# Kernel tuning notes

Hardware: AMD Instinct MI355X
Metric: run time of the kernel (lower is better)

Reference implementation:

```python
import jax, jax.numpy as jnp
import numpy as np

N_ATOMS = 300000
N_COLS = 8
VOCAB = 4096      # nn.Embedding(4096, per_col_dim)
D_COL = 32        # per_col_dim
HID = 256         # hidden_size
N_BONDS = 320000
B_GRAPHS = 6000
ATOMS_PER_GRAPH = 50
STEPS = 3
SENTINEL = 999999999


def _linear_params(key, fan_in, fan_out):
    lim = 1.0 / np.sqrt(fan_in)
    kw, kb = jax.random.split(key)
    W = jax.random.uniform(kw, (fan_out, fan_in), minval=-lim, maxval=lim, dtype=jnp.float32)
    b = jax.random.uniform(kb, (fan_out,), minval=-lim, maxval=lim, dtype=jnp.float32)
    return W, b


def setup_inputs() -> dict:
    key = jax.random.key(0)
    ks = jax.random.split(key, 8)
    a_features = jax.random.randint(ks[0], (N_ATOMS, N_COLS), 0, VOCAB, dtype=jnp.int32)
    uv = jax.random.randint(ks[1], (N_BONDS, 2), 0, N_ATOMS, dtype=jnp.int32)
    bextra = jax.random.randint(ks[2], (N_BONDS, 1), 0, 16, dtype=jnp.int32)
    b_features = jnp.concatenate([uv, bextra], axis=1)
    # contiguous equal-length scopes: graph i owns atoms [i*50, i*50+50)
    starts = np.arange(B_GRAPHS, dtype=np.int32) * ATOMS_PER_GRAPH
    lengths = np.full(B_GRAPHS, ATOMS_PER_GRAPH, dtype=np.int32)
    a_scopes = jnp.asarray(np.stack([starts, lengths], axis=1))
    emb_weights = jax.random.normal(ks[3], (N_COLS, VOCAB, D_COL), dtype=jnp.float32) * 0.02
    W_in, b_in = _linear_params(ks[4], D_COL, HID)
    W_self, b_self = _linear_params(ks[5], HID, HID)
    W_neigh, b_neigh = _linear_params(ks[6], HID, HID)
    W_out, b_out = _linear_params(ks[7], HID, HID)
    return {
        'a_features': a_features, 'b_features': b_features, 'a_scopes': a_scopes,
        'emb_weights': emb_weights,
        'W_in': W_in, 'b_in': b_in,
        'W_self': W_self, 'b_self': b_self,
        'W_neigh': W_neigh, 'b_neigh': b_neigh,
        'W_out': W_out, 'b_out': b_out,
    }


def reference(a_features, b_features, a_scopes, emb_weights,
              W_in, b_in, W_self, b_self, W_neigh, b_neigh, W_out, b_out):
    # --- per-column embedding lookup, summed over columns ---
    idx = jnp.remainder(a_features, VOCAB)
    idx = jnp.where(a_features >= SENTINEL, 0, idx)          # sentinel -> index 0
    x = jnp.zeros((a_features.shape[0], D_COL), dtype=emb_weights.dtype)
    for c in range(N_COLS):                                   # fixed small loop over columns
        x = x + emb_weights[c][idx[:, c]]
    h = x @ W_in.T + b_in                                     # [N, HID]
    # --- undirected edges -> two directed edge lists ---
    u = b_features[:, 0]
    v = b_features[:, 1]
    src = jnp.concatenate([u, v], axis=0)
    dst = jnp.concatenate([v, u], axis=0)
    # --- message passing steps ---
    for _ in range(STEPS):
        agg = jnp.zeros_like(h).at[dst].add(h[src])           # scatter-add neighbor sum
        h = jax.nn.relu(h @ W_self.T + b_self + agg @ W_neigh.T + b_neigh)
    h = h @ W_out.T + b_out
    # --- per-graph mean pooling over contiguous scopes ---
    lengths = a_scopes[:, 1]
    seg_ids = jnp.repeat(jnp.arange(a_scopes.shape[0]), lengths,
                         total_repeat_length=h.shape[0])
    sums = jax.ops.segment_sum(h, seg_ids, num_segments=a_scopes.shape[0])
    denom = jnp.maximum(lengths, 1).astype(h.dtype)[:, None]
    return sums / denom
```

## Files before the change

### kernel.cpp

```cpp
#include <hip/hip_runtime.h>

#define NATOMS 300000
#define NCOLS 8
#define VOCABSZ 4096
#define DCOL 32
#define HIDDIM 256
#define NBONDS 320000
#define NGRAPHS 6000
#define NSTEPS 3

constexpr int MP = 300032;
constexpr int MTILES64 = MP / 64;

typedef _Float16 f16;
typedef _Float16 f16x4 __attribute__((ext_vector_type(4)));
typedef _Float16 f16x8 __attribute__((ext_vector_type(8)));
typedef float f32x4 __attribute__((ext_vector_type(4)));

constexpr float LO_SCALE = 2048.0f;
constexpr float INV_LO   = 1.0f / 2048.0f;

__device__ __forceinline__ void split2(float x, f16& h, f16& l) {
    h = (f16)x;
    l = (f16)((x - (float)h) * LO_SCALE);
}

__device__ __forceinline__ int swz(int row, int q) {
    return (row * 4 + (q ^ ((row >> 1) & 3))) * 8;
}

static void* g_pool = nullptr;
__attribute__((constructor)) static void alloc_pool() {
    void* p = nullptr;
    if (hipMalloc(&p, (size_t)1024 * 1024 * 1024) == hipSuccess) {
        hipMemset(p, 0, (size_t)1024 * 1024 * 1024);
        g_pool = p;
    }
}

__global__ void fill_kernel(float* out, float v, int n) {
    int i = blockIdx.x * blockDim.x + threadIdx.x;
    if (i < n) out[i] = v;
}

__global__ void build_edges_kernel(const int* __restrict__ bf, int* __restrict__ esrc,
                                   int* __restrict__ nxt, int* head) {
    int e = blockIdx.x * blockDim.x + threadIdx.x;
    if (e >= 2 * NBONDS) return;
    int src, dst;
    if (e < NBONDS) { src = bf[e * 3 + 0]; dst = bf[e * 3 + 1]; }
    else { int i = e - NBONDS; src = bf[i * 3 + 1]; dst = bf[i * 3 + 0]; }
    esrc[e] = src;
    nxt[e] = atomicExch(&head[dst], e);
}

__global__ void wsplit_kernel(const float* __restrict__ W, f16* __restrict__ Wh,
                              f16* __restrict__ Wl, int n) {
    int i = blockIdx.x * blockDim.x + threadIdx.x;
    if (i >= n) return;
    split2(W[i], Wh[i], Wl[i]);
}

__global__ void bsum_kernel(const float* __restrict__ a, const float* __restrict__ b,
                            float* __restrict__ o) {
    int i = threadIdx.x;
    o[i] = a[i] + b[i];
}

__global__ void embed_kernel(const int* __restrict__ af, const float* __restrict__ emb,
                             f16* __restrict__ xh, f16* __restrict__ xl) {
    int gid = blockIdx.x * blockDim.x + threadIdx.x;
    int i = gid >> 5, k = gid & 31;
    if (i >= NATOMS) return;
    float s = 0.0f;
#pragma unroll
    for (int c = 0; c < NCOLS; c++) {
        int v = af[i * NCOLS + c];
        int idx = v & (VOCABSZ - 1);
        if (v >= 999999999) idx = 0;
        s += emb[((size_t)c * VOCABSZ + idx) * DCOL + k];
    }
    split2(s, xh[(size_t)i * DCOL + k], xl[(size_t)i * DCOL + k]);
}

__global__ void agg_kernel(const f16* __restrict__ Ahi, const f16* __restrict__ Alo,
                           f16* __restrict__ Ghi, f16* __restrict__ Glo,
                           const int* __restrict__ head, const int* __restrict__ nxt,
                           const int* __restrict__ esrc) {
    int wid = (blockIdx.x * blockDim.x + threadIdx.x) >> 6;
    int lane = threadIdx.x & 63;
    if (wid >= NATOMS) return;
    float4 sh = make_float4(0.f, 0.f, 0.f, 0.f);
    float4 sl = make_float4(0.f, 0.f, 0.f, 0.f);
    int e = head[wid];
    while (e >= 0) {
        int src = esrc[e];
        const f16x4 vh = *(const f16x4*)(Ahi + (size_t)src * HIDDIM + lane * 4);
        const f16x4 vl = *(const f16x4*)(Alo + (size_t)src * HIDDIM + lane * 4);
        sh.x += (float)vh.x; sh.y += (float)vh.y; sh.z += (float)vh.z; sh.w += (float)vh.w;
        sl.x += (float)vl.x; sl.y += (float)vl.y; sl.z += (float)vl.z; sl.w += (float)vl.w;
        e = nxt[e];
    }
    float4 s;
    s.x = sh.x + sl.x * INV_LO; s.y = sh.y + sl.y * INV_LO;
    s.z = sh.z + sl.z * INV_LO; s.w = sh.w + sl.w * INV_LO;
    f16 h0, l0, h1, l1, h2, l2, h3, l3;
    split2(s.x, h0, l0); split2(s.y, h1, l1);
    split2(s.z, h2, l2); split2(s.w, h3, l3);
    f16x4 oh, ol;
    oh.x = h0; oh.y = h1; oh.z = h2; oh.w = h3;
    ol.x = l0; ol.y = l1; ol.z = l2; ol.w = l3;
    *(f16x4*)(Ghi + (size_t)wid * HIDDIM + lane * 4) = oh;
    *(f16x4*)(Glo + (size_t)wid * HIDDIM + lane * 4) = ol;
}

template <bool HAS_A2, bool RELU, int K>
__global__ __launch_bounds__(256, 2) void mfma_gemm(
    const f16* __restrict__ A1h, const f16* __restrict__ A1l,
    const f16* __restrict__ A2h, const f16* __restrict__ A2l,
    const f16* __restrict__ B1h, const f16* __restrict__ B1l,
    const f16* __restrict__ B2h, const f16* __restrict__ B2l,
    const float* __restrict__ bias,
    f16* __restrict__ Chi, f16* __restrict__ Clo) {
    __shared__ __align__(16) f16 sAh[64 * 32];
    __shared__ __align__(16) f16 sAl[64 * 32];
    __shared__ __align__(16) f16 sBh[256 * 32];
    __shared__ __align__(16) f16 sBl[256 * 32];

    const int t = threadIdx.x;
    const int m0 = blockIdx.x * 64;
    const int lane = t & 63;
    const int wid = t >> 6;
    const int wn = wid * 64;
    const int quad = lane >> 4;
    const int l16 = lane & 15;

    f32x4 acch[4][4], accl[4][4];
#pragma unroll
    for (int a = 0; a < 4; a++)
#pragma unroll
        for (int b = 0; b < 4; b++) {
            acch[a][b] = (f32x4){0.f, 0.f, 0.f, 0.f};
            accl[a][b] = (f32x4){0.f, 0.f, 0.f, 0.f};
        }

    const int NMAT = HAS_A2 ? 2 : 1;
    for (int kb = 0; kb < K; kb += 32) {
        for (int mat = 0; mat < NMAT; mat++) {
            const f16* Ah = (mat == 0) ? A1h : A2h;
            const f16* Al = (mat == 0) ? A1l : A2l;
            const f16* Bh = (mat == 0) ? B1h : B2h;
            const f16* Bl = (mat == 0) ? B1l : B2l;
            __syncthreads();
            {
                const int r = t >> 2, q = t & 3;
                const int dst = swz(r, q);
                *(int4*)(sAh + dst) = *(const int4*)(Ah + (size_t)(m0 + r) * K + kb + q * 8);
                *(int4*)(sAl + dst) = *(const int4*)(Al + (size_t)(m0 + r) * K + kb + q * 8);
            }
#pragma unroll
            for (int i = 0; i < 4; i++) {
                const int u = t + 256 * i;
                const int r = u >> 2, q = u & 3;
                const int dst = swz(r, q);
                *(int4*)(sBh + dst) = *(const int4*)(Bh + (size_t)r * K + kb + q * 8);
                *(int4*)(sBl + dst) = *(const int4*)(Bl + (size_t)r * K + kb + q * 8);
            }
            __syncthreads();

            f16x8 fah[4], fal[4];
#pragma unroll
            for (int mt = 0; mt < 4; mt++) {
                const int src = swz(mt * 16 + l16, quad);
                fah[mt] = *(const f16x8*)(sAh + src);
                fal[mt] = *(const f16x8*)(sAl + src);
            }
#pragma unroll
            for (int nt = 0; nt < 4; nt++) {
                const int src = swz(wn + nt * 16 + l16, quad);
                const f16x8 bh = *(const f16x8*)(sBh + src);
                const f16x8 bl = *(const f16x8*)(sBl + src);
#pragma unroll
                for (int mt = 0; mt < 4; mt++) {
                    acch[mt][nt] = __builtin_amdgcn_mfma_f32_16x16x32_f16(fah[mt], bh, acch[mt][nt], 0, 0, 0);
                    accl[mt][nt] = __builtin_amdgcn_mfma_f32_16x16x32_f16(fah[mt], bl, accl[mt][nt], 0, 0, 0);
                    accl[mt][nt] = __builtin_amdgcn_mfma_f32_16x16x32_f16(fal[mt], bh, accl[mt][nt], 0, 0, 0);
                }
            }
        }
    }

#pragma unroll
    for (int mt = 0; mt < 4; mt++) {
#pragma unroll
        for (int nt = 0; nt < 4; nt++) {
            const int col = wn + nt * 16 + l16;
            const float bv = bias[col];
#pragma unroll
            for (int r = 0; r < 4; r++) {
                const int row = m0 + mt * 16 + quad * 4 + r;
                float v = acch[mt][nt][r] + accl[mt][nt][r] * INV_LO + bv;
                if (RELU) v = fmaxf(v, 0.f);
                f16 hi, lo;
                split2(v, hi, lo);
                Chi[(size_t)row * HIDDIM + col] = hi;
                Clo[(size_t)row * HIDDIM + col] = lo;
            }
        }
    }
}

__global__ void readout_kernel(const f16* __restrict__ Hhi, const f16* __restrict__ Hlo,
                               const int* __restrict__ scopes, float* __restrict__ out) {
    int g = blockIdx.x;
    int n = threadIdx.x;
    int start = scopes[g * 2 + 0];
    int len = scopes[g * 2 + 1];
    float s = 0.f;
    for (int j = 0; j < len; j++) {
        size_t o = (size_t)(start + j) * HIDDIM + n;
        s += (float)Hhi[o] + (float)Hlo[o] * INV_LO;
    }
    int d = len > 1 ? len : 1;
    out[(size_t)g * HIDDIM + n] = s / (float)d;
}

extern "C" void kernel_launch(void* const* d_in, const int* in_sizes, int n_in,
                              void* d_out, int out_size, void* d_ws, size_t ws_size,
                              hipStream_t stream) {
    const int* a_features = (const int*)d_in[0];
    const int* b_features = (const int*)d_in[1];
    const int* a_scopes   = (const int*)d_in[2];
    const float* emb      = (const float*)d_in[3];
    const float* W_in     = (const float*)d_in[4];
    const float* b_in     = (const float*)d_in[5];
    const float* W_self   = (const float*)d_in[6];
    const float* b_self   = (const float*)d_in[7];
    const float* W_neigh  = (const float*)d_in[8];
    const float* b_neigh  = (const float*)d_in[9];
    const float* W_out    = (const float*)d_in[10];
    const float* b_out    = (const float*)d_in[11];

    if (g_pool == nullptr) {
        fill_kernel<<<(out_size + 255) / 256, 256, 0, stream>>>(
            (float*)d_out, 77777.0f, out_size);
        return;
    }

    f16* p = (f16*)g_pool;
    const size_t HB = (size_t)MP * HIDDIM;
    f16* hAhi = p;            f16* hAlo = p + HB;
    f16* hBhi = p + 2 * HB;   f16* hBlo = p + 3 * HB;
    f16* hChi = p + 4 * HB;   f16* hClo = p + 5 * HB;
    f16* xhi  = p + 6 * HB;
    f16* xlo  = xhi + (size_t)MP * DCOL;
    f16* Winh = xlo + (size_t)MP * DCOL;
    f16* Winl = Winh + HIDDIM * DCOL;
    f16* Wsh  = Winl + HIDDIM * DCOL;
    f16* Wsl  = Wsh + HIDDIM * HIDDIM;
    f16* Wnh  = Wsl + HIDDIM * HIDDIM;
    f16* Wnl  = Wnh + HIDDIM * HIDDIM;
    f16* Woh  = Wnl + HIDDIM * HIDDIM;
    f16* Wol  = Woh + HIDDIM * HIDDIM;
    float* bsum = (float*)(Wol + HIDDIM * HIDDIM);
    int* esrc = (int*)(bsum + HIDDIM);
    int* nxt  = esrc + 2 * NBONDS;
    int* head = nxt + 2 * NBONDS;

    constexpr int NPAD = MP - NATOMS;

    hipMemsetAsync(head, 0xFF, (size_t)MP * sizeof(int), stream);
    build_edges_kernel<<<(2 * NBONDS + 255) / 256, 256, 0, stream>>>(b_features, esrc, nxt, head);
    wsplit_kernel<<<(HIDDIM * DCOL + 255) / 256, 256, 0, stream>>>(W_in, Winh, Winl, HIDDIM * DCOL);
    wsplit_kernel<<<(HIDDIM * HIDDIM + 255) / 256, 256, 0, stream>>>(W_self, Wsh, Wsl, HIDDIM * HIDDIM);
    wsplit_kernel<<<(HIDDIM * HIDDIM + 255) / 256, 256, 0, stream>>>(W_neigh, Wnh, Wnl, HIDDIM * HIDDIM);
    wsplit_kernel<<<(HIDDIM * HIDDIM + 255) / 256, 256, 0, stream>>>(W_out, Woh, Wol, HIDDIM * HIDDIM);
    bsum_kernel<<<1, HIDDIM, 0, stream>>>(b_self, b_neigh, bsum);

    constexpr int PADF = NPAD * HIDDIM / 2;
    fill_kernel<<<(PADF + 255) / 256, 256, 0, stream>>>((float*)(hAhi + (size_t)NATOMS * HIDDIM), 0.f, PADF);
    fill_kernel<<<(PADF + 255) / 256, 256, 0, stream>>>((float*)(hAlo + (size_t)NATOMS * HIDDIM), 0.f, PADF);
    fill_kernel<<<(PADF + 255) / 256, 256, 0, stream>>>((float*)(hBhi + (size_t)NATOMS * HIDDIM), 0.f, PADF);
    fill_kernel<<<(PADF + 255) / 256, 256, 0, stream>>>((float*)(hBlo + (size_t)NATOMS * HIDDIM), 0.f, PADF);
    fill_kernel<<<(PADF + 255) / 256, 256, 0, stream>>>((float*)(hChi + (size_t)NATOMS * HIDDIM), 0.f, PADF);
    fill_kernel<<<(PADF + 255) / 256, 256, 0, stream>>>((float*)(hClo + (size_t)NATOMS * HIDDIM), 0.f, PADF);
    constexpr int PADX = NPAD * DCOL / 2;
    fill_kernel<<<(PADX + 255) / 256, 256, 0, stream>>>((float*)(xhi + (size_t)NATOMS * DCOL), 0.f, PADX);
    fill_kernel<<<(PADX + 255) / 256, 256, 0, stream>>>((float*)(xlo + (size_t)NATOMS * DCOL), 0.f, PADX);

    embed_kernel<<<(NATOMS * DCOL + 255) / 256, 256, 0, stream>>>(a_features, emb, xhi, xlo);
    mfma_gemm<false, false, DCOL><<<MTILES64, 256, 0, stream>>>(
        xhi, xlo, nullptr, nullptr, Winh, Winl, nullptr, nullptr, b_in, hAhi, hAlo);

    f16 *h_hi = hAhi, *h_lo = hAlo;
    f16 *g_hi = hBhi, *g_lo = hBlo;
    f16 *n_hi = hChi, *n_lo = hClo;
    for (int s = 0; s < NSTEPS; s++) {
        agg_kernel<<<NATOMS / 4, 256, 0, stream>>>(h_hi, h_lo, g_hi, g_lo, head, nxt, esrc);
        mfma_gemm<true, true, HIDDIM><<<MTILES64, 256, 0, stream>>>(
            h_hi, h_lo, g_hi, g_lo, Wsh, Wsl, Wnh, Wnl, bsum, n_hi, n_lo);
        f16* t1 = h_hi; f16* t2 = h_lo;
        h_hi = n_hi; h_lo = n_lo;
        n_hi = g_hi; n_lo = g_lo;
        g_hi = t1;   g_lo = t2;
    }

    mfma_gemm<false, false, HIDDIM><<<MTILES64, 256, 0, stream>>>(
        h_hi, h_lo, nullptr, nullptr, Woh, Wol, nullptr, nullptr, b_out, g_hi, g_lo);
    readout_kernel<<<NGRAPHS, 256, 0, stream>>>(g_hi, g_lo, a_scopes, (float*)d_out);
}
```

Baseline: 2.173 ms.

## Use 128-row GEMM tiles and a single accumulator with unscaled low parts

The MFMA GEMM tile grows from 64 to 128 rows, with the four waves arranged 2x2 (64 rows by 128 columns each), so each staged B tile of the weights is reused across twice as many rows. The split-f16 scheme also changes: the low part is no longer scaled by 2048, the weights are prescaled by 128 instead, and all three MFMA products go into one accumulator, which halves accumulator registers. The bigger tile means more LDS and 32 accumulator vectors per wave, which may lower occupancy. Dropping the low-part scaling risks underflow of small residuals in f16 and so reduces accuracy.

```diff
diff --git a/kernel.cpp b/kernel.cpp
--- a/kernel.cpp
+++ b/kernel.cpp
@@ -10,19 +10,19 @@
 #define NSTEPS 3
 
 constexpr int MP = 300032;
-constexpr int MTILES64 = MP / 64;
+constexpr int MTILES128 = MP / 128;
 
 typedef _Float16 f16;
 typedef _Float16 f16x4 __attribute__((ext_vector_type(4)));
 typedef _Float16 f16x8 __attribute__((ext_vector_type(8)));
 typedef float f32x4 __attribute__((ext_vector_type(4)));
 
-constexpr float LO_SCALE = 2048.0f;
-constexpr float INV_LO   = 1.0f / 2048.0f;
+constexpr float W_SCALE = 128.0f;
+constexpr float INV_W   = 1.0f / 128.0f;
 
 __device__ __forceinline__ void split2(float x, f16& h, f16& l) {
     h = (f16)x;
-    l = (f16)((x - (float)h) * LO_SCALE);
+    l = (f16)(x - (float)h);
 }
 
 __device__ __forceinline__ int swz(int row, int q) {
@@ -58,7 +58,7 @@
                               f16* __restrict__ Wl, int n) {
     int i = blockIdx.x * blockDim.x + threadIdx.x;
     if (i >= n) return;
-    split2(W[i], Wh[i], Wl[i]);
+    split2(W[i] * W_SCALE, Wh[i], Wl[i]);
 }
 
 __global__ void bsum_kernel(const float* __restrict__ a, const float* __restrict__ b,
@@ -102,8 +102,8 @@
         e = nxt[e];
     }
     float4 s;
-    s.x = sh.x + sl.x * INV_LO; s.y = sh.y + sl.y * INV_LO;
-    s.z = sh.z + sl.z * INV_LO; s.w = sh.w + sl.w * INV_LO;
+    s.x = sh.x + sl.x; s.y = sh.y + sl.y;
+    s.z = sh.z + sl.z; s.w = sh.w + sl.w;
     f16 h0, l0, h1, l1, h2, l2, h3, l3;
     split2(s.x, h0, l0); split2(s.y, h1, l1);
     split2(s.z, h2, l2); split2(s.w, h3, l3);
@@ -122,27 +122,25 @@
     const f16* __restrict__ B2h, const f16* __restrict__ B2l,
     const float* __restrict__ bias,
     f16* __restrict__ Chi, f16* __restrict__ Clo) {
-    __shared__ __align__(16) f16 sAh[64 * 32];
-    __shared__ __align__(16) f16 sAl[64 * 32];
+    __shared__ __align__(16) f16 sAh[128 * 32];
+    __shared__ __align__(16) f16 sAl[128 * 32];
     __shared__ __align__(16) f16 sBh[256 * 32];
     __shared__ __align__(16) f16 sBl[256 * 32];
 
     const int t = threadIdx.x;
-    const int m0 = blockIdx.x * 64;
+    const int m0 = blockIdx.x * 128;
     const int lane = t & 63;
     const int wid = t >> 6;
-    const int wn = wid * 64;
+    const int wm = (wid >> 1) * 64;
+    const int wn = (wid & 1) * 128;
     const int quad = lane >> 4;
     const int l16 = lane & 15;
 
-    f32x4 acch[4][4], accl[4][4];
+    f32x4 acc[4][8];
 #pragma unroll
     for (int a = 0; a < 4; a++)
 #pragma unroll
-        for (int b = 0; b < 4; b++) {
-            acch[a][b] = (f32x4){0.f, 0.f, 0.f, 0.f};
-            accl[a][b] = (f32x4){0.f, 0.f, 0.f, 0.f};
-        }
+        for (int b = 0; b < 8; b++) acc[a][b] = (f32x4){0.f, 0.f, 0.f, 0.f};
 
     const int NMAT = HAS_A2 ? 2 : 1;
     for (int kb = 0; kb < K; kb += 32) {
@@ -152,8 +150,10 @@
             const f16* Bh = (mat == 0) ? B1h : B2h;
             const f16* Bl = (mat == 0) ? B1l : B2l;
             __syncthreads();
-            {
-                const int r = t >> 2, q = t & 3;
+#pragma unroll
+            for (int i = 0; i < 2; i++) {
+                const int u = t + 256 * i;
+                const int r = u >> 2, q = u & 3;
                 const int dst = swz(r, q);
                 *(int4*)(sAh + dst) = *(const int4*)(Ah + (size_t)(m0 + r) * K + kb + q * 8);
                 *(int4*)(sAl + dst) = *(const int4*)(Al + (size_t)(m0 + r) * K + kb + q * 8);
@@ -171,20 +171,20 @@
             f16x8 fah[4], fal[4];
 #pragma unroll
             for (int mt = 0; mt < 4; mt++) {
-                const int src = swz(mt * 16 + l16, quad);
+                const int src = swz(wm + mt * 16 + l16, quad);
                 fah[mt] = *(const f16x8*)(sAh + src);
                 fal[mt] = *(const f16x8*)(sAl + src);
             }
 #pragma unroll
-            for (int nt = 0; nt < 4; nt++) {
+            for (int nt = 0; nt < 8; nt++) {
                 const int src = swz(wn + nt * 16 + l16, quad);
                 const f16x8 bh = *(const f16x8*)(sBh + src);
                 const f16x8 bl = *(const f16x8*)(sBl + src);
 #pragma unroll
                 for (int mt = 0; mt < 4; mt++) {
-                    acch[mt][nt] = __builtin_amdgcn_mfma_f32_16x16x32_f16(fah[mt], bh, acch[mt][nt], 0, 0, 0);
-                    accl[mt][nt] = __builtin_amdgcn_mfma_f32_16x16x32_f16(fah[mt], bl, accl[mt][nt], 0, 0, 0);
-                    accl[mt][nt] = __builtin_amdgcn_mfma_f32_16x16x32_f16(fal[mt], bh, accl[mt][nt], 0, 0, 0);
+                    acc[mt][nt] = __builtin_amdgcn_mfma_f32_16x16x32_f16(fah[mt], bh, acc[mt][nt], 0, 0, 0);
+                    acc[mt][nt] = __builtin_amdgcn_mfma_f32_16x16x32_f16(fah[mt], bl, acc[mt][nt], 0, 0, 0);
+                    acc[mt][nt] = __builtin_amdgcn_mfma_f32_16x16x32_f16(fal[mt], bh, acc[mt][nt], 0, 0, 0);
                 }
             }
         }
@@ -193,13 +193,13 @@
 #pragma unroll
     for (int mt = 0; mt < 4; mt++) {
 #pragma unroll
-        for (int nt = 0; nt < 4; nt++) {
+        for (int nt = 0; nt < 8; nt++) {
             const int col = wn + nt * 16 + l16;
             const float bv = bias[col];
 #pragma unroll
             for (int r = 0; r < 4; r++) {
-                const int row = m0 + mt * 16 + quad * 4 + r;
-                float v = acch[mt][nt][r] + accl[mt][nt][r] * INV_LO + bv;
+                const int row = m0 + wm + mt * 16 + quad * 4 + r;
+                float v = acc[mt][nt][r] * INV_W + bv;
                 if (RELU) v = fmaxf(v, 0.f);
                 f16 hi, lo;
                 split2(v, hi, lo);
@@ -219,7 +219,7 @@
     float s = 0.f;
     for (int j = 0; j < len; j++) {
         size_t o = (size_t)(start + j) * HIDDIM + n;
-        s += (float)Hhi[o] + (float)Hlo[o] * INV_LO;
+        s += (float)Hhi[o] + (float)Hlo[o];
     }
     int d = len > 1 ? len : 1;
     out[(size_t)g * HIDDIM + n] = s / (float)d;
@@ -289,7 +289,7 @@
     fill_kernel<<<(PADX + 255) / 256, 256, 0, stream>>>((float*)(xlo + (size_t)NATOMS * DCOL), 0.f, PADX);
 
     embed_kernel<<<(NATOMS * DCOL + 255) / 256, 256, 0, stream>>>(a_features, emb, xhi, xlo);
-    mfma_gemm<false, false, DCOL><<<MTILES64, 256, 0, stream>>>(
+    mfma_gemm<false, false, DCOL><<<MTILES128, 256, 0, stream>>>(
         xhi, xlo, nullptr, nullptr, Winh, Winl, nullptr, nullptr, b_in, hAhi, hAlo);
 
     f16 *h_hi = hAhi, *h_lo = hAlo;
@@ -297,7 +297,7 @@
     f16 *n_hi = hChi, *n_lo = hClo;
     for (int s = 0; s < NSTEPS; s++) {
         agg_kernel<<<NATOMS / 4, 256, 0, stream>>>(h_hi, h_lo, g_hi, g_lo, head, nxt, esrc);
-        mfma_gemm<true, true, HIDDIM><<<MTILES64, 256, 0, stream>>>(
+        mfma_gemm<true, true, HIDDIM><<<MTILES128, 256, 0, stream>>>(
             h_hi, h_lo, g_hi, g_lo, Wsh, Wsl, Wnh, Wnl, bsum, n_hi, n_lo);
         f16* t1 = h_hi; f16* t2 = h_lo;
         h_hi = n_hi; h_lo = n_lo;
@@ -305,7 +305,7 @@
         g_hi = t1;   g_lo = t2;
     }
 
-    mfma_gemm<false, false, HIDDIM><<<MTILES64, 256, 0, stream>>>(
+    mfma_gemm<false, false, HIDDIM><<<MTILES128, 256, 0, stream>>>(
         h_hi, h_lo, nullptr, nullptr, Woh, Wol, nullptr, nullptr, b_out, g_hi, g_lo);
     readout_kernel<<<NGRAPHS, 256, 0, stream>>>(g_hi, g_lo, a_scopes, (float*)d_out);
 }
```

Result: slower. 2.541 ms (+16.9%).
